# Kernel tuning notes

Measured on AMD Instinct MI355X. Metric: run time of the kernel, lower is better.

The kernel has to match this reference:

```python
import jax, jax.numpy as jnp
import numpy as np

BS, QLEN, KLEN = 2, 64, 64
N_HEADS, D_KV = 8, 64
INNER = N_HEADS * D_KV  # 512
VOCAB = 4096


def _layernorm(x, g, b, eps=1e-6):
    m = jnp.mean(x, axis=-1, keepdims=True)
    v = jnp.mean(jnp.square(x - m), axis=-1, keepdims=True)
    return (x - m) * jax.lax.rsqrt(v + eps) * g + b


def _l2norm(x, eps=1e-12):
    sq = jnp.sum(jnp.square(x), axis=-1, keepdims=True)
    return x * jax.lax.rsqrt(jnp.maximum(sq, eps))


def setup_inputs() -> dict:
    key = jax.random.key(0)
    ks = jax.random.split(key, 8)
    d = {
        'query': jax.random.normal(ks[0], (BS, QLEN, INNER), jnp.float32),
        'key': jax.random.normal(ks[1], (BS, KLEN, INNER), jnp.float32),
        'q_position_embeddings': jax.random.normal(ks[2], (BS, QLEN, INNER), jnp.float32),
        'k_position_embeddings': jax.random.normal(ks[3], (BS, KLEN, INNER), jnp.float32),
        'wi_w': jax.random.normal(ks[4], (2 * INNER, INNER), jnp.float32) / np.sqrt(2 * INNER),
        'vq_dict': jax.random.normal(ks[5], (VOCAB, D_KV), jnp.float32) * np.sqrt(2.0 / (VOCAB + D_KV)),
        'vq_ln_g': jnp.ones((D_KV,), jnp.float32),
        'vq_ln_b': jnp.zeros((D_KV,), jnp.float32),
        'vq_o_w': jax.random.normal(ks[6], (D_KV, D_KV), jnp.float32) / np.sqrt(D_KV),
        'ln_g': jnp.ones((D_KV,), jnp.float32),
        'ln_b': jnp.zeros((D_KV,), jnp.float32),
    }
    return d


def reference(query, key, q_position_embeddings, k_position_embeddings,
              wi_w, vq_dict, vq_ln_g, vq_ln_b, vq_o_w, ln_g, ln_b):
    bs, qlen, dim = query.shape
    klen = key.shape[1]

    q = query + q_position_embeddings
    k = key + k_position_embeddings
    # wi(concat([q, 0])) == q @ wi_w[:dim]; wi(concat([0, k])) == k @ wi_w[dim:]
    q_proj = jnp.einsum('bqd,de->bqe', q, wi_w[:dim])   # [bs, qlen, inner]
    k_proj = jnp.einsum('bkd,de->bke', k, wi_w[dim:])   # [bs, klen, inner]

    # pairwise outer sum -> [bs, qlen, klen, inner] -> tokens of size d_kv
    rcr = q_proj[:, :, None, :] + k_proj[:, None, :, :]
    y = rcr.reshape(bs, qlen * klen * N_HEADS, D_KV)

    # --- VectorQuantizer (eval mode: no dropout, loss = 0) ---
    y_n = _l2norm(y)
    d_n = _l2norm(vq_dict)
    sim = jnp.einsum('bnd,vd->bnv', y_n, d_n)           # [bs, N, vocab]
    word_idx = jnp.argmax(sim, axis=-1)                 # [bs, N] int
    word_sim = jnp.max(sim, axis=-1)                    # [bs, N]
    z = vq_dict[word_idx]                               # gather
    emb = jax.lax.stop_gradient(z - y) + y              # straight-through
    emb = _layernorm(emb, vq_ln_g, vq_ln_b)
    emb = jnp.einsum('bnd,de->bne', emb, vq_o_w)

    r3 = emb.reshape(bs, qlen, klen, N_HEADS, D_KV)
    r3_scores = word_sim.reshape(bs, qlen, klen, N_HEADS, 1)
    out_ids = word_idx.reshape(bs, qlen, klen, N_HEADS, 1)

    r3_weighted = jnp.mean(r3 * r3_scores, axis=2)      # [bs, qlen, n_heads, d_kv]
    r3_weighted = jnp.transpose(r3_weighted, (0, 2, 1, 3))  # [bs, n_heads, qlen, d_kv]
    r3_weighted = _layernorm(r3_weighted, ln_g, ln_b)
    return r3_weighted, out_ids, r3_scores
```

## Files before the change

### kernel.cpp

```cpp
#include <hip/hip_runtime.h>
#include <math.h>

#define BS 2
#define QLEN 64
#define KLEN 64
#define NH 8
#define DKV 64
#define INNER 512
#define VOCAB 4096
#define CHUNKV 64
#define RS 130
#define BUFD (CHUNKV * RS)

typedef double vdbl4 __attribute__((ext_vector_type(4)));
typedef double vdbl2 __attribute__((ext_vector_type(2)));


__global__ __launch_bounds__(256) void k_prep(
    const float* __restrict__ q_in, const float* __restrict__ k_in,
    const float* __restrict__ qpe, const float* __restrict__ kpe,
    const float* __restrict__ wi,
    const float* __restrict__ vq, const float* __restrict__ g,
    const float* __restrict__ bta, const float* __restrict__ ow,
    double* __restrict__ qp, double* __restrict__ kp,
    double* __restrict__ dnt, float* __restrict__ E,
    unsigned long long* __restrict__ bestf)
{
    __shared__ double S[1600];
    __shared__ float Osh[4096];
    int bid = blockIdx.x;
    int t = threadIdx.x;

    if (bid < 1024) {
        int side = bid >> 9;
        int b    = (bid >> 8) & 1;
        int rp   = (bid >> 3) & 31;
        int cb   = bid & 7;
        const float* xin = side ? k_in : q_in;
        const float* pin = side ? kpe : qpe;
        double* outp = side ? kp : qp;
        int wrow0 = side ? INNER : 0;
        int r0 = rp * 2;
        double* xs = S;
        double* red = S + 1024;
        for (int i = t; i < 2 * INNER; i += 256) {
            int rr = i >> 9, dd = i & 511;
            int gidx = (b * 64 + r0 + rr) * INNER + dd;
            xs[rr * INNER + dd] = (double)xin[gidx] + (double)pin[gidx];
        }
        __syncthreads();
        int col = cb * 64 + (t & 63);
        int dh = t >> 6;
        double a0 = 0.0, a1 = 0.0;
        #pragma unroll 8
        for (int d = dh * 128; d < dh * 128 + 128; ++d) {
            double w = (double)wi[(size_t)(wrow0 + d) * INNER + col];
            a0 = fma(xs[d], w, a0);
            a1 = fma(xs[INNER + d], w, a1);
        }
        red[(dh * 2 + 0) * 64 + (t & 63)] = a0;
        red[(dh * 2 + 1) * 64 + (t & 63)] = a1;
        __syncthreads();
        if (t < 128) {
            int rr = t >> 6, c2 = t & 63;
            double s = (red[(0 * 2 + rr) * 64 + c2] + red[(1 * 2 + rr) * 64 + c2])
                     + (red[(2 * 2 + rr) * 64 + c2] + red[(3 * 2 + rr) * 64 + c2]);
            outp[(size_t)(b * 64 + r0 + rr) * INNER + cb * 64 + c2] = s;
        }
    } else {
        int db = bid - 1024;
        if (db < 256) bestf[db * 256 + t] = 0ull;
        double* Lsh = S;
        double* Dsh = S + 256;
        int vb = db * 4;
        int wv = t >> 6, lane = t & 63;
        for (int i = t; i < 4096; i += 256) Osh[i] = ow[i];
        int v = vb + wv;
        double z = (double)vq[v * DKV + lane];
        double s2 = z * z, s1 = z;
        for (int m = 32; m >= 1; m >>= 1) { s2 += __shfl_xor(s2, m); s1 += __shfl_xor(s1, m); }
        Dsh[lane * 5 + wv] = z * (1.0 / sqrt(fmax(s2, 1e-12)));
        double mean = s1 * (1.0 / 64.0);
        double d0 = z - mean;
        double vv2 = d0 * d0;
        for (int m = 32; m >= 1; m >>= 1) vv2 += __shfl_xor(vv2, m);
        vv2 *= (1.0 / 64.0);
        Lsh[wv * 64 + lane] = d0 * (1.0 / sqrt(vv2 + 1e-6)) * (double)g[lane] + (double)bta[lane];
        __syncthreads();
        double c0 = 0.0, c1 = 0.0, c2 = 0.0, c3 = 0.0;
        #pragma unroll 4
        for (int gg = 0; gg < 16; ++gg) {
            int jj = gg * 4;
            c0 = fma(Lsh[wv * 64 + jj + 0], (double)Osh[(jj + 0) * 64 + lane], c0);
            c1 = fma(Lsh[wv * 64 + jj + 1], (double)Osh[(jj + 1) * 64 + lane], c1);
            c2 = fma(Lsh[wv * 64 + jj + 2], (double)Osh[(jj + 2) * 64 + lane], c2);
            c3 = fma(Lsh[wv * 64 + jj + 3], (double)Osh[(jj + 3) * 64 + lane], c3);
        }
        E[v * DKV + lane] = (float)((c0 + c1) + (c2 + c3));
        {
            int j = t >> 2, vloc = t & 3;
            dnt[(size_t)j * VOCAB + vb + vloc] = Dsh[j * 5 + vloc];
        }
    }
}

__global__ __launch_bounds__(1024, 4) void k_simscan(
    const double* __restrict__ qp, const double* __restrict__ kp,
    const double* __restrict__ dnt,
    unsigned long long* __restrict__ bestf)
{
    int bid = blockIdx.x;
    int bh = bid & 15, cg = bid >> 4;
    int b = bh >> 3, h = bh & 7;
    int t = threadIdx.x;
    int w = t >> 6, l = t & 63;

    __shared__ double S[2 * BUFD];

    int asub = l >> 4;
    int lrow = l & 15;
    bool isprod = (w < 8);

    int drow[4], dcol[4];
    {
        vdbl4 prow = (vdbl4){0.0, 0.0, 0.0, 0.0};
        vdbl4 pcol = (vdbl4){0.0, 0.0, 0.0, 0.0};
        double a_row = (asub == 0) ? (double)lrow : 0.0;
        double b_one = (asub == 0) ? 1.0 : 0.0;
        double a_one = (asub == 0) ? 1.0 : 0.0;
        double b_col = (asub == 0) ? (double)lrow : 0.0;
        prow = __builtin_amdgcn_mfma_f64_16x16x4f64(a_row, b_one, prow, 0, 0, 0);
        pcol = __builtin_amdgcn_mfma_f64_16x16x4f64(a_one, b_col, pcol, 0, 0, 0);
        #pragma unroll
        for (int r = 0; r < 4; ++r) { drow[r] = (int)prow[r]; dcol[r] = (int)pcol[r]; }
    }

    double afr[16];
    if (isprod) {
        const double* src = (w < 4) ? qp : kp;
        int arow = (w & 3) * 16 + lrow;
        #pragma unroll
        for (int ks = 0; ks < 16; ++ks)
            afr[ks] = src[(size_t)(b * 64 + arow) * INNER + h * 64 + ks * 4 + asub];
    }

    int ci = t - 512;
    int qg = ci & 15, kg = (ci >> 4) & 31;
    double best[4][2];
    #pragma unroll
    for (int i = 0; i < 4; ++i)
        #pragma unroll
        for (int j = 0; j < 2; ++j) best[i][j] = 0.0;

    for (int step = 0; step < 5; ++step) {
        if (isprod && step < 4) {
            int v0 = (cg * 4 + step) * CHUNKV;
            double* buf = S + (step & 1) * BUFD;
            vdbl4 acc[4];
            #pragma unroll
            for (int vt = 0; vt < 4; ++vt) acc[vt] = (vdbl4){0.0, 0.0, 0.0, 0.0};
            size_t base = (size_t)asub * VOCAB + v0 + lrow;
            double bcur[4], bnext[4];
            #pragma unroll
            for (int vt = 0; vt < 4; ++vt) bcur[vt] = dnt[base + vt * 16];
            #pragma unroll
            for (int ks = 0; ks < 16; ++ks) {
                if (ks < 15) {
                    size_t krow = base + (size_t)((ks + 1) * 4) * VOCAB;
                    #pragma unroll
                    for (int vt = 0; vt < 4; ++vt) bnext[vt] = dnt[krow + vt * 16];
                }
                #pragma unroll
                for (int vt = 0; vt < 4; ++vt)
                    acc[vt] = __builtin_amdgcn_mfma_f64_16x16x4f64(
                        afr[ks], bcur[vt], acc[vt], 0, 0, 0);
                if (ks < 15) {
                    #pragma unroll
                    for (int vt = 0; vt < 4; ++vt) bcur[vt] = bnext[vt];
                }
            }
            bool isq = (w < 4);
            #pragma unroll
            for (int vt = 0; vt < 4; ++vt)
                #pragma unroll
                for (int r = 0; r < 4; ++r) {
                    int vl = vt * 16 + dcol[r];
                    int grow = (w & 3) * 16 + drow[r];
                    int slot = isq ? ((grow & 15) * 4 + (grow >> 4))
                                   : (64 + (grow & 31) * 2 + (grow >> 5));
                    unsigned long long code =
                        (unsigned long long)((4095 - (v0 + vl)) << 1);
                    double s = fma(acc[vt][r], 1.0 / 64.0, 1.5);
                    unsigned long long bb2 = __double_as_longlong(s) & ~0x1FFFull;
                    if (isq) bb2 |= code;
                    buf[vl * RS + slot] = __longlong_as_double(bb2);
                }
        }
        if (!isprod && step >= 1) {
            double* buf = S + ((step - 1) & 1) * BUFD;
            #pragma unroll 2
            for (int v = 0; v < CHUNKV; ++v) {
                vdbl2 q01 = *(const vdbl2*)&buf[v * RS + qg * 4];
                vdbl2 q23 = *(const vdbl2*)&buf[v * RS + qg * 4 + 2];
                vdbl2 k01 = *(const vdbl2*)&buf[v * RS + 64 + kg * 2];
                best[0][0] = fmax(best[0][0], q01[0] + k01[0]);
                best[0][1] = fmax(best[0][1], q01[0] + k01[1]);
                best[1][0] = fmax(best[1][0], q01[1] + k01[0]);
                best[1][1] = fmax(best[1][1], q01[1] + k01[1]);
                best[2][0] = fmax(best[2][0], q23[0] + k01[0]);
                best[2][1] = fmax(best[2][1], q23[0] + k01[1]);
                best[3][0] = fmax(best[3][0], q23[1] + k01[0]);
                best[3][1] = fmax(best[3][1], q23[1] + k01[1]);
            }
        }
        if (step < 4) __syncthreads();
    }

    if (!isprod) {
        #pragma unroll
        for (int i = 0; i < 4; ++i)
            #pragma unroll
            for (int j = 0; j < 2; ++j) {
                int q = qg + 16 * i, k = kg + 32 * j;
                atomicMax(&bestf[((size_t)bh * 64 + q) * 64 + k],
                          (unsigned long long)__double_as_longlong(best[i][j]));
            }
    }
}

__global__ __launch_bounds__(256) void k_combine(
    const unsigned long long* __restrict__ bestf,
    const double* __restrict__ qp, const double* __restrict__ kp,
    const float* __restrict__ E,
    const float* __restrict__ lng, const float* __restrict__ lnb,
    float* __restrict__ out)
{
    int bid = blockIdx.x;
    int bh = bid & 15, q = bid >> 4;
    int b = bh >> 3, h = bh & 7;
    int t = threadIdx.x;
    int w = t >> 6, lane = t & 63;

    __shared__ double qrow[64];
    __shared__ double gpart[4][64];
    __shared__ double knpart[4][64];
    __shared__ double qnpart[4];
    __shared__ float  ws_l[64];
    __shared__ int    idx_l[64];
    __shared__ float  epart[4][64];

    if (t < 64) qrow[t] = qp[(size_t)(b * 64 + q) * INNER + h * 64 + t];
    __syncthreads();

    {
        const double* krow = kp + (size_t)(b * 64 + lane) * INNER + h * 64 + w * 16;
        double gd = 0.0, kn = 0.0;
        #pragma unroll
        for (int i = 0; i < 16; ++i) {
            double xk = krow[i];
            gd = fma(qrow[w * 16 + i], xk, gd);
            kn = fma(xk, xk, kn);
        }
        gpart[w][lane] = gd;
        knpart[w][lane] = kn;
        if (lane == 0) {
            double qn = 0.0;
            #pragma unroll
            for (int i = 0; i < 16; ++i) { double xq = qrow[w * 16 + i]; qn = fma(xq, xq, qn); }
            qnpart[w] = qn;
        }
    }
    __syncthreads();

    if (w == 0) {
        int k = lane;
        double gdot = (gpart[0][k] + gpart[1][k]) + (gpart[2][k] + gpart[3][k]);
        double kn2  = (knpart[0][k] + knpart[1][k]) + (knpart[2][k] + knpart[3][k]);
        double qn2  = (qnpart[0] + qnpart[1]) + (qnpart[2] + qnpart[3]);
        unsigned long long bb = bestf[((size_t)bh * 64 + q) * 64 + k];
        int vidx = 4095 - (int)(bb & 0xFFFull);
        double sval = __longlong_as_double(bb & ~0x1FFFull);
        double tru = (sval - 3.0) * 64.0;
        double n2 = qn2 + kn2 + 2.0 * gdot;
        double wsim = tru * (1.0 / sqrt(fmax(n2, 1e-12)));
        size_t oidx = ((size_t)(b * QLEN + q) * KLEN + k) * NH + h;
        out[65536 + oidx] = (float)vidx;
        out[131072 + oidx] = (float)wsim;
        ws_l[k] = (float)wsim;
        idx_l[k] = vidx;
    }
    __syncthreads();

    {
        int d = lane;
        float acc = 0.0f;
        #pragma unroll 4
        for (int k2 = w * 16; k2 < w * 16 + 16; ++k2)
            acc += E[idx_l[k2] * DKV + d] * ws_l[k2];
        epart[w][d] = acc;
    }
    __syncthreads();

    if (w == 0) {
        int d = lane;
        float acc = ((epart[0][d] + epart[1][d]) + (epart[2][d] + epart[3][d])) * (1.0f / 64.0f);
        float mean = acc;
        for (int m = 32; m >= 1; m >>= 1) mean += __shfl_xor(mean, m);
        mean *= (1.0f / 64.0f);
        float dv = acc - mean;
        float var = dv * dv;
        for (int m = 32; m >= 1; m >>= 1) var += __shfl_xor(var, m);
        var *= (1.0f / 64.0f);
        float o = dv * rsqrtf(var + 1e-6f) * lng[d] + lnb[d];
        out[(((size_t)b * NH + h) * QLEN + q) * DKV + d] = o;
    }
}

extern "C" void kernel_launch(void* const* d_in, const int* in_sizes, int n_in,
                              void* d_out, int out_size, void* d_ws, size_t ws_size,
                              hipStream_t stream) {
    const float* query = (const float*)d_in[0];
    const float* key   = (const float*)d_in[1];
    const float* qpe   = (const float*)d_in[2];
    const float* kpe   = (const float*)d_in[3];
    const float* wi    = (const float*)d_in[4];
    const float* vq    = (const float*)d_in[5];
    const float* vqg   = (const float*)d_in[6];
    const float* vqb   = (const float*)d_in[7];
    const float* ow    = (const float*)d_in[8];
    const float* lng   = (const float*)d_in[9];
    const float* lnb   = (const float*)d_in[10];
    float* out = (float*)d_out;

    char* ws = (char*)d_ws;
    double* qp  = (double*)(ws + 0);
    double* kp  = (double*)(ws + 524288);
    double* dnt = (double*)(ws + 1048576);
    float*  E   = (float*) (ws + 3145728);
    unsigned long long* bestf = (unsigned long long*)(ws + 4194304);

    k_prep   <<<2048, 256, 0, stream>>>(query, key, qpe, kpe, wi, vq, vqg, vqb, ow,
                                        qp, kp, dnt, E, bestf);
    k_simscan<<<256, 1024, 0, stream>>>(qp, kp, dnt, bestf);
    k_combine<<<1024, 256, 0, stream>>>(bestf, qp, kp, E, lng, lnb, out);
}
```

Measured before the change: 154.2 us.

## Split prep kernel and compute projections with FP64 MFMA tiles

Splits the combined prep kernel into a projection kernel and a dictionary-normalisation kernel. The projection now uses FP64 MFMA 16x16x4 instructions over 16-row tiles held in padded shared memory, and register-double-buffers the weight loads, in place of scalar FMA with a shared-memory reduction. The extra kernel launch and the small 64-block grid may leave much of the GPU idle, and each block now re-reads the weight columns.

```diff
diff --git a/kernel.cpp b/kernel.cpp
--- a/kernel.cpp
+++ b/kernel.cpp
@@ -16,91 +16,120 @@
 typedef double vdbl2 __attribute__((ext_vector_type(2)));
 
 
-__global__ __launch_bounds__(256) void k_prep(
+__global__ __launch_bounds__(256) void k_proj(
     const float* __restrict__ q_in, const float* __restrict__ k_in,
     const float* __restrict__ qpe, const float* __restrict__ kpe,
     const float* __restrict__ wi,
+    double* __restrict__ qp, double* __restrict__ kp)
+{
+    __shared__ double xs[16 * 513];
+    int bid = blockIdx.x;
+    int sb  = bid >> 4;
+    int side = sb >> 1, b = sb & 1;
+    int rt  = (bid >> 2) & 3;
+    int cgp = bid & 3;
+    const float* xin = side ? k_in : q_in;
+    const float* pin = side ? kpe : qpe;
+    double* outp = side ? kp : qp;
+    int wrow0 = side ? INNER : 0;
+    int t = threadIdx.x;
+    int w = t >> 6, l = t & 63;
+    int lrow = l & 15, asub = l >> 4;
+
+    int drow[4], dcol[4];
+    {
+        vdbl4 prow = (vdbl4){0.0, 0.0, 0.0, 0.0};
+        vdbl4 pcol = (vdbl4){0.0, 0.0, 0.0, 0.0};
+        double a_row = (asub == 0) ? (double)lrow : 0.0;
+        double b_one = (asub == 0) ? 1.0 : 0.0;
+        double a_one = (asub == 0) ? 1.0 : 0.0;
+        double b_col = (asub == 0) ? (double)lrow : 0.0;
+        prow = __builtin_amdgcn_mfma_f64_16x16x4f64(a_row, b_one, prow, 0, 0, 0);
+        pcol = __builtin_amdgcn_mfma_f64_16x16x4f64(a_one, b_col, pcol, 0, 0, 0);
+        #pragma unroll
+        for (int r = 0; r < 4; ++r) { drow[r] = (int)prow[r]; dcol[r] = (int)pcol[r]; }
+    }
+
+    for (int i = t; i < 16 * 512; i += 256) {
+        int row = i >> 9, dd = i & 511;
+        int g = (b * 64 + rt * 16 + row) * INNER + dd;
+        xs[row * 513 + dd] = (double)xin[g] + (double)pin[g];
+    }
+    __syncthreads();
+
+    int cb2 = cgp * 128 + w * 32 + lrow;
+    vdbl4 acc0 = (vdbl4){0.0, 0.0, 0.0, 0.0};
+    vdbl4 acc1 = (vdbl4){0.0, 0.0, 0.0, 0.0};
+
+    double bf[2][2];
+    #pragma unroll
+    for (int p = 0; p < 2; ++p) {
+        const float* wk = wi + (size_t)(wrow0 + p * 4 + asub) * INNER + cb2;
+        bf[p][0] = (double)wk[0];
+        bf[p][1] = (double)wk[16];
+    }
+    #pragma unroll 2
+    for (int ks = 0; ks < 128; ++ks) {
+        double a = xs[lrow * 513 + ks * 4 + asub];
+        double b0 = bf[ks & 1][0], b1 = bf[ks & 1][1];
+        if (ks < 126) {
+            const float* wk = wi + (size_t)(wrow0 + (ks + 2) * 4 + asub) * INNER + cb2;
+            bf[ks & 1][0] = (double)wk[0];
+            bf[ks & 1][1] = (double)wk[16];
+        }
+        acc0 = __builtin_amdgcn_mfma_f64_16x16x4f64(a, b0, acc0, 0, 0, 0);
+        acc1 = __builtin_amdgcn_mfma_f64_16x16x4f64(a, b1, acc1, 0, 0, 0);
+    }
+
+    #pragma unroll
+    for (int r = 0; r < 4; ++r) {
+        size_t rowoff = (size_t)(b * 64 + rt * 16 + drow[r]) * INNER + cgp * 128 + w * 32;
+        outp[rowoff + dcol[r]] = acc0[r];
+        outp[rowoff + 16 + dcol[r]] = acc1[r];
+    }
+}
+
+__global__ __launch_bounds__(256) void k_dict(
     const float* __restrict__ vq, const float* __restrict__ g,
     const float* __restrict__ bta, const float* __restrict__ ow,
-    double* __restrict__ qp, double* __restrict__ kp,
     double* __restrict__ dnt, float* __restrict__ E,
     unsigned long long* __restrict__ bestf)
 {
-    __shared__ double S[1600];
+    __shared__ double S[576];
     __shared__ float Osh[4096];
-    int bid = blockIdx.x;
+    int db = blockIdx.x;
     int t = threadIdx.x;
-
-    if (bid < 1024) {
-        int side = bid >> 9;
-        int b    = (bid >> 8) & 1;
-        int rp   = (bid >> 3) & 31;
-        int cb   = bid & 7;
-        const float* xin = side ? k_in : q_in;
-        const float* pin = side ? kpe : qpe;
-        double* outp = side ? kp : qp;
-        int wrow0 = side ? INNER : 0;
-        int r0 = rp * 2;
-        double* xs = S;
-        double* red = S + 1024;
-        for (int i = t; i < 2 * INNER; i += 256) {
-            int rr = i >> 9, dd = i & 511;
-            int gidx = (b * 64 + r0 + rr) * INNER + dd;
-            xs[rr * INNER + dd] = (double)xin[gidx] + (double)pin[gidx];
-        }
-        __syncthreads();
-        int col = cb * 64 + (t & 63);
-        int dh = t >> 6;
-        double a0 = 0.0, a1 = 0.0;
-        #pragma unroll 8
-        for (int d = dh * 128; d < dh * 128 + 128; ++d) {
-            double w = (double)wi[(size_t)(wrow0 + d) * INNER + col];
-            a0 = fma(xs[d], w, a0);
-            a1 = fma(xs[INNER + d], w, a1);
-        }
-        red[(dh * 2 + 0) * 64 + (t & 63)] = a0;
-        red[(dh * 2 + 1) * 64 + (t & 63)] = a1;
-        __syncthreads();
-        if (t < 128) {
-            int rr = t >> 6, c2 = t & 63;
-            double s = (red[(0 * 2 + rr) * 64 + c2] + red[(1 * 2 + rr) * 64 + c2])
-                     + (red[(2 * 2 + rr) * 64 + c2] + red[(3 * 2 + rr) * 64 + c2]);
-            outp[(size_t)(b * 64 + r0 + rr) * INNER + cb * 64 + c2] = s;
-        }
-    } else {
-        int db = bid - 1024;
-        if (db < 256) bestf[db * 256 + t] = 0ull;
-        double* Lsh = S;
-        double* Dsh = S + 256;
-        int vb = db * 4;
-        int wv = t >> 6, lane = t & 63;
-        for (int i = t; i < 4096; i += 256) Osh[i] = ow[i];
-        int v = vb + wv;
-        double z = (double)vq[v * DKV + lane];
-        double s2 = z * z, s1 = z;
-        for (int m = 32; m >= 1; m >>= 1) { s2 += __shfl_xor(s2, m); s1 += __shfl_xor(s1, m); }
-        Dsh[lane * 5 + wv] = z * (1.0 / sqrt(fmax(s2, 1e-12)));
-        double mean = s1 * (1.0 / 64.0);
-        double d0 = z - mean;
-        double vv2 = d0 * d0;
-        for (int m = 32; m >= 1; m >>= 1) vv2 += __shfl_xor(vv2, m);
-        vv2 *= (1.0 / 64.0);
-        Lsh[wv * 64 + lane] = d0 * (1.0 / sqrt(vv2 + 1e-6)) * (double)g[lane] + (double)bta[lane];
-        __syncthreads();
-        double c0 = 0.0, c1 = 0.0, c2 = 0.0, c3 = 0.0;
-        #pragma unroll 4
-        for (int gg = 0; gg < 16; ++gg) {
-            int jj = gg * 4;
-            c0 = fma(Lsh[wv * 64 + jj + 0], (double)Osh[(jj + 0) * 64 + lane], c0);
-            c1 = fma(Lsh[wv * 64 + jj + 1], (double)Osh[(jj + 1) * 64 + lane], c1);
-            c2 = fma(Lsh[wv * 64 + jj + 2], (double)Osh[(jj + 2) * 64 + lane], c2);
-            c3 = fma(Lsh[wv * 64 + jj + 3], (double)Osh[(jj + 3) * 64 + lane], c3);
-        }
-        E[v * DKV + lane] = (float)((c0 + c1) + (c2 + c3));
-        {
-            int j = t >> 2, vloc = t & 3;
-            dnt[(size_t)j * VOCAB + vb + vloc] = Dsh[j * 5 + vloc];
-        }
+    if (db < 256) bestf[db * 256 + t] = 0ull;
+    double* Lsh = S;
+    double* Dsh = S + 256;
+    int vb = db * 4;
+    int wv = t >> 6, lane = t & 63;
+    for (int i = t; i < 4096; i += 256) Osh[i] = ow[i];
+    int v = vb + wv;
+    double z = (double)vq[v * DKV + lane];
+    double s2 = z * z, s1 = z;
+    for (int m = 32; m >= 1; m >>= 1) { s2 += __shfl_xor(s2, m); s1 += __shfl_xor(s1, m); }
+    Dsh[lane * 5 + wv] = z * (1.0 / sqrt(fmax(s2, 1e-12)));
+    double mean = s1 * (1.0 / 64.0);
+    double d0 = z - mean;
+    double vv2 = d0 * d0;
+    for (int m = 32; m >= 1; m >>= 1) vv2 += __shfl_xor(vv2, m);
+    vv2 *= (1.0 / 64.0);
+    Lsh[wv * 64 + lane] = d0 * (1.0 / sqrt(vv2 + 1e-6)) * (double)g[lane] + (double)bta[lane];
+    __syncthreads();
+    double c0 = 0.0, c1 = 0.0, c2 = 0.0, c3 = 0.0;
+    #pragma unroll 4
+    for (int gg = 0; gg < 16; ++gg) {
+        int jj = gg * 4;
+        c0 = fma(Lsh[wv * 64 + jj + 0], (double)Osh[(jj + 0) * 64 + lane], c0);
+        c1 = fma(Lsh[wv * 64 + jj + 1], (double)Osh[(jj + 1) * 64 + lane], c1);
+        c2 = fma(Lsh[wv * 64 + jj + 2], (double)Osh[(jj + 2) * 64 + lane], c2);
+        c3 = fma(Lsh[wv * 64 + jj + 3], (double)Osh[(jj + 3) * 64 + lane], c3);
+    }
+    E[v * DKV + lane] = (float)((c0 + c1) + (c2 + c3));
+    {
+        int j = t >> 2, vloc = t & 3;
+        dnt[(size_t)j * VOCAB + vb + vloc] = Dsh[j * 5 + vloc];
     }
 }
 
@@ -339,8 +368,8 @@
     float*  E   = (float*) (ws + 3145728);
     unsigned long long* bestf = (unsigned long long*)(ws + 4194304);
 
-    k_prep   <<<2048, 256, 0, stream>>>(query, key, qpe, kpe, wi, vq, vqg, vqb, ow,
-                                        qp, kp, dnt, E, bestf);
+    k_proj   <<<64, 256, 0, stream>>>(query, key, qpe, kpe, wi, qp, kp);
+    k_dict   <<<1024, 256, 0, stream>>>(vq, vqg, vqb, ow, dnt, E, bestf);
     k_simscan<<<256, 1024, 0, stream>>>(qp, kp, dnt, bestf);
     k_combine<<<1024, 256, 0, stream>>>(bestf, qp, kp, E, lng, lnb, out);
 }
```

Result: slower. 198.3 us (+28.6%).
